# Kernel tuning notes

Measured on AMD Instinct MI355X. Metric: run time of the kernel, lower is better.

The kernel has to match this reference:

```python
import jax, jax.numpy as jnp
import numpy as np

B = 2097152   # batch
Z = 16        # z_dim
K = 64        # num_hidden_nodes


def setup_inputs() -> dict:
    key = jax.random.key(0)
    k1, k2, k3, k4, k5 = jax.random.split(key, 5)
    return {
        "z": jax.random.normal(k1, (B, Z), dtype=jnp.float32),
        "a_0": jax.random.normal(k2, (1,), dtype=jnp.float32),
        "bk": jax.random.normal(k3, (K,), dtype=jnp.float32),
        "ck": jax.random.normal(k4, (K, Z), dtype=jnp.float32),
        "dk": jax.random.normal(k5, (K,), dtype=jnp.float32),
    }


def reference(z, a_0, bk, ck, dk):
    # Vectorized over the batch: y[b] = a_0 + sum_k bk[k] * tanh((ck @ z[b])[k] + dk[k])
    h = jnp.tanh(jnp.einsum("bz,kz->bk", z, ck) + dk)  # [B, K]
    y = a_0 + h @ bk                                     # [B]
    return y[:, None]                                     # [B, 1]
```

## Files before the change

kernel.cpp:

```cpp
#include <hip/hip_runtime.h>
#include <stdint.h>

typedef __attribute__((ext_vector_type(8)))  short  short8;
typedef __attribute__((ext_vector_type(8)))  __bf16 bf16x8;
typedef __attribute__((ext_vector_type(16))) float  floatx16;
typedef __attribute__((ext_vector_type(4)))  float  floatx4;
typedef __attribute__((ext_vector_type(2)))  float  float2v;
typedef __attribute__((ext_vector_type(4)))  uint32_t uint4v;

union Frag { short8 s; bf16x8 v; uint4v d; };
union FU   { float f; uint32_t u; };

__device__ __forceinline__ short f2bf(float f) {
    FU x; x.f = f;
    uint32_t r = x.u + 0x7fffu + ((x.u >> 16) & 1u);
    return (short)(r >> 16);
}

__device__ __forceinline__ uint32_t pack_bf2(float lo, float hi) {
    FU a, b; a.f = lo; b.f = hi;
    return __builtin_amdgcn_perm(b.u + 0x8000u, a.u + 0x8000u, 0x07060302u);
}

__device__ __forceinline__ float fexp2(float x) { return __builtin_amdgcn_exp2f(x); }
__device__ __forceinline__ float frcp(float x)  { return __builtin_amdgcn_rcpf(x); }
__device__ __forceinline__ float fclamp(float x, float lo, float hi) {
#if __has_builtin(__builtin_amdgcn_fmed3f)
    return __builtin_amdgcn_fmed3f(x, lo, hi);
#else
    return fminf(fmaxf(x, lo), hi);
#endif
}

__device__ __forceinline__ float2v tpair(float a, float b) {
    float2v t;
    t.x = fexp2(fclamp(a, -30.0f, 30.0f));
    t.y = fexp2(fclamp(b, -30.0f, 30.0f));
    return t + 1.0f;
}

__global__ __launch_bounds__(256) void mave_kernel(
    const float* __restrict__ z,
    const float* __restrict__ a0,
    const float* __restrict__ bk,
    const float* __restrict__ ck,
    const float* __restrict__ dk,
    float* __restrict__ out,
    int ntiles)
{
    const int lane = threadIdx.x & 63;
    const int m    = lane & 31;
    const int g    = lane >> 5;
    const float S  = 2.885390081777927f;

    Frag af0, af1;
    {
        const float* c0 = ck + m * 16 + g * 8;
        const float* c1 = c0 + 32 * 16;
        #pragma unroll
        for (int e = 0; e < 8; ++e) {
            af0.s[e] = f2bf(c0[e] * S);
            af1.s[e] = f2bf(c1[e] * S);
        }
    }

    floatx16 cinit0, cinit1;
    float2v nb2[16];
    #pragma unroll
    for (int r = 0; r < 16; ++r) {
        int n = (r & 3) + 8 * (r >> 2) + 4 * g;
        cinit0[r] = S * dk[n];
        cinit1[r] = S * dk[n + 32];
        nb2[r].x = -2.0f * bk[n];
        nb2[r].y = -2.0f * bk[n + 32];
    }

    float base = a0[0];
    for (int k = 0; k < 64; ++k) base += bk[k];

    const int wid = (int)((blockIdx.x * blockDim.x + threadIdx.x) >> 6);
    const int nw  = (int)((gridDim.x * blockDim.x) >> 6);
    const int per  = (ntiles + nw - 1) / nw;
    const int tbeg = wid * per;
    const int tend = (tbeg + per < ntiles) ? tbeg + per : ntiles;
    if (tbeg >= tend) return;

    floatx4 a0v, a1v, b0v, b1v;
    {
        const float* zp = z + (size_t)(tbeg * 32 + m) * 16 + g * 8;
        a0v = *(const floatx4*)zp; a1v = *(const floatx4*)(zp + 4);
        int t1i = (tbeg + 1 < tend) ? tbeg + 1 : tbeg;
        const float* zq = z + (size_t)(t1i * 32 + m) * 16 + g * 8;
        b0v = *(const floatx4*)zq; b1v = *(const floatx4*)(zq + 4);
    }

    #pragma unroll 1
    for (int t = tbeg; t < tend; t += 2) {
        Frag bfr;
        bfr.d[0] = pack_bf2(a0v.x, a0v.y); bfr.d[1] = pack_bf2(a0v.z, a0v.w);
        bfr.d[2] = pack_bf2(a1v.x, a1v.y); bfr.d[3] = pack_bf2(a1v.z, a1v.w);
        if (t + 2 < tend) {
            const float* zp = z + (size_t)((t + 2) * 32 + m) * 16 + g * 8;
            a0v = *(const floatx4*)zp; a1v = *(const floatx4*)(zp + 4);
        }
        floatx16 acc0 = __builtin_amdgcn_mfma_f32_32x32x16_bf16(af0.v, bfr.v, cinit0, 0, 0, 0);
        floatx16 acc1 = __builtin_amdgcn_mfma_f32_32x32x16_bf16(af1.v, bfr.v, cinit1, 0, 0, 0);

        float2v Ya = {0.0f, 0.0f}, Yb = {0.0f, 0.0f};
        #pragma unroll
        for (int r = 0; r < 16; r += 4) {
            float2v T0 = tpair(acc0[r+0], acc1[r+0]);
            float2v T1 = tpair(acc0[r+1], acc1[r+1]);
            float2v T2 = tpair(acc0[r+2], acc1[r+2]);
            float2v T3 = tpair(acc0[r+3], acc1[r+3]);
            float2v P01 = T0 * T1, P23 = T2 * T3, P = P01 * P23;
            float2v R; R.x = frcp(P.x); R.y = frcp(P.y);
            float2v n01 = nb2[r+0] * T1 + nb2[r+1] * T0;
            float2v n23 = nb2[r+2] * T3 + nb2[r+3] * T2;
            float2v num = n01 * P23 + n23 * P01;
            if (r & 4) Yb += num * R; else Ya += num * R;
        }
        float2v Yv = Ya + Yb;
        float y = Yv.x + Yv.y;
        y += __shfl_xor(y, 32, 64);
        if (g == 0) out[t * 32 + m] = base + y;

        if (t + 1 < tend) {
            Frag bf2;
            bf2.d[0] = pack_bf2(b0v.x, b0v.y); bf2.d[1] = pack_bf2(b0v.z, b0v.w);
            bf2.d[2] = pack_bf2(b1v.x, b1v.y); bf2.d[3] = pack_bf2(b1v.z, b1v.w);
            if (t + 3 < tend) {
                const float* zp = z + (size_t)((t + 3) * 32 + m) * 16 + g * 8;
                b0v = *(const floatx4*)zp; b1v = *(const floatx4*)(zp + 4);
            }
            floatx16 ac0 = __builtin_amdgcn_mfma_f32_32x32x16_bf16(af0.v, bf2.v, cinit0, 0, 0, 0);
            floatx16 ac1 = __builtin_amdgcn_mfma_f32_32x32x16_bf16(af1.v, bf2.v, cinit1, 0, 0, 0);

            float2v Yc = {0.0f, 0.0f}, Yd = {0.0f, 0.0f};
            #pragma unroll
            for (int r = 0; r < 16; r += 4) {
                float2v T0 = tpair(ac0[r+0], ac1[r+0]);
                float2v T1 = tpair(ac0[r+1], ac1[r+1]);
                float2v T2 = tpair(ac0[r+2], ac1[r+2]);
                float2v T3 = tpair(ac0[r+3], ac1[r+3]);
                float2v P01 = T0 * T1, P23 = T2 * T3, P = P01 * P23;
                float2v R; R.x = frcp(P.x); R.y = frcp(P.y);
                float2v n01 = nb2[r+0] * T1 + nb2[r+1] * T0;
                float2v n23 = nb2[r+2] * T3 + nb2[r+3] * T2;
                float2v num = n01 * P23 + n23 * P01;
                if (r & 4) Yd += num * R; else Yc += num * R;
            }
            float2v Yv2 = Yc + Yd;
            float y2 = Yv2.x + Yv2.y;
            y2 += __shfl_xor(y2, 32, 64);
            if (g == 0) out[(t + 1) * 32 + m] = base + y2;
        }
    }
}

extern "C" void kernel_launch(void* const* d_in, const int* in_sizes, int n_in,
                              void* d_out, int out_size, void* d_ws, size_t ws_size,
                              hipStream_t stream) {
    const float* z  = (const float*)d_in[0];
    const float* a0 = (const float*)d_in[1];
    const float* bk = (const float*)d_in[2];
    const float* ck = (const float*)d_in[3];
    const float* dk = (const float*)d_in[4];
    float* out = (float*)d_out;

    const int B      = in_sizes[0] / 16;
    const int ntiles = B / 32;

    dim3 grid(2048), block(256);
    hipLaunchKernelGGL(mave_kernel, grid, block, 0, stream,
                       z, a0, bk, ck, dk, out, ntiles);
}
```

Measured before the change: 205.1 us.

## Deepen z prefetch to a 4-slot register ring and pack bk weights as bf16

Replaces the two-tile manual software pipeline with a 4-deep register ring of prefetched z tiles, processed in a loop unrolled by 4, so more global loads are in flight per wave. The -2*bk coefficients are stored as packed bf16 pairs and unpacked with shifts and masks to free registers for the deeper ring. This trades extra ALU unpack work and reduced coefficient precision for better latency hiding. Prefetch indices are clamped to the last tile, so tail iterations issue redundant loads.

```diff
diff --git a/kernel.cpp b/kernel.cpp
--- a/kernel.cpp
+++ b/kernel.cpp
@@ -65,14 +65,13 @@
     }
 
     floatx16 cinit0, cinit1;
-    float2v nb2[16];
+    uint32_t nbp[16];
     #pragma unroll
     for (int r = 0; r < 16; ++r) {
         int n = (r & 3) + 8 * (r >> 2) + 4 * g;
         cinit0[r] = S * dk[n];
         cinit1[r] = S * dk[n + 32];
-        nb2[r].x = -2.0f * bk[n];
-        nb2[r].y = -2.0f * bk[n + 32];
+        nbp[r] = pack_bf2(-2.0f * bk[n], -2.0f * bk[n + 32]);
     }
 
     float base = a0[0];
@@ -84,25 +83,35 @@
     const int tbeg = wid * per;
     const int tend = (tbeg + per < ntiles) ? tbeg + per : ntiles;
     if (tbeg >= tend) return;
+    const int tlast = tend - 1;
 
-    floatx4 a0v, a1v, b0v, b1v;
-    {
-        const float* zp = z + (size_t)(tbeg * 32 + m) * 16 + g * 8;
-        a0v = *(const floatx4*)zp; a1v = *(const floatx4*)(zp + 4);
-        int t1i = (tbeg + 1 < tend) ? tbeg + 1 : tbeg;
-        const float* zq = z + (size_t)(t1i * 32 + m) * 16 + g * 8;
-        b0v = *(const floatx4*)zq; b1v = *(const floatx4*)(zq + 4);
+    const float* zb = z + (size_t)m * 16 + g * 8;
+    floatx4 ring[4][2];
+    #pragma unroll
+    for (int i = 0; i < 4; ++i) {
+        int ti = tbeg + i; if (ti > tlast) ti = tlast;
+        const float* zp = zb + (size_t)ti * 512;
+        ring[i][0] = *(const floatx4*)zp;
+        ring[i][1] = *(const floatx4*)(zp + 4);
     }
 
-    #pragma unroll 1
-    for (int t = tbeg; t < tend; t += 2) {
+    #pragma unroll 4
+    for (int t = tbeg; t < tend; ++t) {
+        const int slot = (t - tbeg) & 3;
+
         Frag bfr;
-        bfr.d[0] = pack_bf2(a0v.x, a0v.y); bfr.d[1] = pack_bf2(a0v.z, a0v.w);
-        bfr.d[2] = pack_bf2(a1v.x, a1v.y); bfr.d[3] = pack_bf2(a1v.z, a1v.w);
-        if (t + 2 < tend) {
-            const float* zp = z + (size_t)((t + 2) * 32 + m) * 16 + g * 8;
-            a0v = *(const floatx4*)zp; a1v = *(const floatx4*)(zp + 4);
+        bfr.d[0] = pack_bf2(ring[slot][0].x, ring[slot][0].y);
+        bfr.d[1] = pack_bf2(ring[slot][0].z, ring[slot][0].w);
+        bfr.d[2] = pack_bf2(ring[slot][1].x, ring[slot][1].y);
+        bfr.d[3] = pack_bf2(ring[slot][1].z, ring[slot][1].w);
+
+        int tf = t + 4; if (tf > tlast) tf = tlast;
+        {
+            const float* zp = zb + (size_t)tf * 512;
+            ring[slot][0] = *(const floatx4*)zp;
+            ring[slot][1] = *(const floatx4*)(zp + 4);
         }
+
         floatx16 acc0 = __builtin_amdgcn_mfma_f32_32x32x16_bf16(af0.v, bfr.v, cinit0, 0, 0, 0);
         floatx16 acc1 = __builtin_amdgcn_mfma_f32_32x32x16_bf16(af1.v, bfr.v, cinit1, 0, 0, 0);
 
@@ -115,8 +124,15 @@
             float2v T3 = tpair(acc0[r+3], acc1[r+3]);
             float2v P01 = T0 * T1, P23 = T2 * T3, P = P01 * P23;
             float2v R; R.x = frcp(P.x); R.y = frcp(P.y);
-            float2v n01 = nb2[r+0] * T1 + nb2[r+1] * T0;
-            float2v n23 = nb2[r+2] * T3 + nb2[r+3] * T2;
+            FU l0, h0, l1, h1, l2, h2, l3, h3;
+            l0.u = nbp[r+0] << 16; h0.u = nbp[r+0] & 0xffff0000u;
+            l1.u = nbp[r+1] << 16; h1.u = nbp[r+1] & 0xffff0000u;
+            l2.u = nbp[r+2] << 16; h2.u = nbp[r+2] & 0xffff0000u;
+            l3.u = nbp[r+3] << 16; h3.u = nbp[r+3] & 0xffff0000u;
+            float2v nb0 = {l0.f, h0.f}, nb1 = {l1.f, h1.f};
+            float2v nb2 = {l2.f, h2.f}, nb3 = {l3.f, h3.f};
+            float2v n01 = nb0 * T1 + nb1 * T0;
+            float2v n23 = nb2 * T3 + nb3 * T2;
             float2v num = n01 * P23 + n23 * P01;
             if (r & 4) Yb += num * R; else Ya += num * R;
         }
@@ -124,37 +140,6 @@
         float y = Yv.x + Yv.y;
         y += __shfl_xor(y, 32, 64);
         if (g == 0) out[t * 32 + m] = base + y;
-
-        if (t + 1 < tend) {
-            Frag bf2;
-            bf2.d[0] = pack_bf2(b0v.x, b0v.y); bf2.d[1] = pack_bf2(b0v.z, b0v.w);
-            bf2.d[2] = pack_bf2(b1v.x, b1v.y); bf2.d[3] = pack_bf2(b1v.z, b1v.w);
-            if (t + 3 < tend) {
-                const float* zp = z + (size_t)((t + 3) * 32 + m) * 16 + g * 8;
-                b0v = *(const floatx4*)zp; b1v = *(const floatx4*)(zp + 4);
-            }
-            floatx16 ac0 = __builtin_amdgcn_mfma_f32_32x32x16_bf16(af0.v, bf2.v, cinit0, 0, 0, 0);
-            floatx16 ac1 = __builtin_amdgcn_mfma_f32_32x32x16_bf16(af1.v, bf2.v, cinit1, 0, 0, 0);
-
-            float2v Yc = {0.0f, 0.0f}, Yd = {0.0f, 0.0f};
-            #pragma unroll
-            for (int r = 0; r < 16; r += 4) {
-                float2v T0 = tpair(ac0[r+0], ac1[r+0]);
-                float2v T1 = tpair(ac0[r+1], ac1[r+1]);
-                float2v T2 = tpair(ac0[r+2], ac1[r+2]);
-                float2v T3 = tpair(ac0[r+3], ac1[r+3]);
-                float2v P01 = T0 * T1, P23 = T2 * T3, P = P01 * P23;
-                float2v R; R.x = frcp(P.x); R.y = frcp(P.y);
-                float2v n01 = nb2[r+0] * T1 + nb2[r+1] * T0;
-                float2v n23 = nb2[r+2] * T3 + nb2[r+3] * T2;
-                float2v num = n01 * P23 + n23 * P01;
-                if (r & 4) Yd += num * R; else Yc += num * R;
-            }
-            float2v Yv2 = Yc + Yd;
-            float y2 = Yv2.x + Yv2.y;
-            y2 += __shfl_xor(y2, 32, 64);
-            if (g == 0) out[(t + 1) * 32 + m] = base + y2;
-        }
     }
 }
 
```

Result: slower. 211.2 us (+3.0%).
